# Kernel tuning notes

Measured on AMD Instinct MI355X. Metric: run time of the kernel, lower is better.

The kernel has to match this reference:

```python
import jax, jax.numpy as jnp
import numpy as np

N_NODES = 100000


def _gcn_layer(x, W, b, src, dst, inv_sqrt_deg):
    # transform first (cheaper when out_dim <= in_dim), then normalized aggregate
    h = x @ W  # [N, out]
    coeff = (inv_sqrt_deg[src] * inv_sqrt_deg[dst])[:, None]  # [E,1] sym norm
    msgs = h[src] * coeff  # [E, out]
    agg = jax.ops.segment_sum(msgs, dst, num_segments=N_NODES)  # [N, out]
    return agg + b


def setup_inputs() -> dict:
    key = jax.random.key(0)
    ks = jax.random.split(key, 8)
    n, e = N_NODES, 1600000
    x = jax.random.normal(ks[0], (n, 256), dtype=jnp.float32)
    src = jax.random.randint(ks[1], (e,), 0, n)
    dst = jax.random.randint(ks[2], (e,), 0, n)
    W1 = jax.random.normal(ks[3], (256, 128), dtype=jnp.float32) * 0.05
    b1 = jax.random.normal(ks[4], (128,), dtype=jnp.float32) * 0.05
    W2 = jax.random.normal(ks[5], (128, 40), dtype=jnp.float32) * 0.05
    b2 = jax.random.normal(ks[6], (40,), dtype=jnp.float32) * 0.05
    return {"x": x, "src": src, "dst": dst, "W1": W1, "b1": b1, "W2": W2, "b2": b2}


def reference(x, src, dst, W1, b1, W2, b2):
    # degree-based symmetric normalization D^{-1/2} A D^{-1/2}
    ones = jnp.ones(src.shape, dtype=x.dtype)
    deg = jax.ops.segment_sum(ones, dst, num_segments=N_NODES)
    inv_sqrt_deg = jnp.where(deg > 0, jax.lax.rsqrt(jnp.maximum(deg, 1.0)), 0.0)
    h = _gcn_layer(x, W1, b1, src, dst, inv_sqrt_deg)
    h = jax.nn.relu(h)
    h = _gcn_layer(h, W2, b2, src, dst, inv_sqrt_deg)
    return h
```

## Files before the change

### kernel.cpp

```cpp
#include <hip/hip_runtime.h>
#include <hip/hip_bf16.h>


#define CHUNK   4096
#define NPB     512
#define NBUCK   196
#define BBCAP   9216

typedef __bf16 bf16x8 __attribute__((ext_vector_type(8)));
typedef float floatx4 __attribute__((ext_vector_type(4)));

__device__ inline unsigned short f2bf(float f) {
    unsigned u = __float_as_uint(f);
    u += 0x7FFF + ((u >> 16) & 1);
    return (unsigned short)(u >> 16);
}
__device__ inline float bflo(unsigned p) { return __uint_as_float(p << 16); }
__device__ inline float bfhi(unsigned p) { return __uint_as_float(p & 0xFFFF0000u); }

__global__ __launch_bounds__(256) void k_f1(const int* __restrict__ src,
                                            const int* __restrict__ dst,
                                            int* __restrict__ gcursor,
                                            unsigned* __restrict__ buckets,
                                            int E, int nchunk,
                                            const float* __restrict__ W1,
                                            unsigned short* __restrict__ w1s,
                                            unsigned* __restrict__ h2z) {
    int t = threadIdx.x;
    if ((int)blockIdx.x >= nchunk) {
        int pb = blockIdx.x - nchunk;
        if (pb == 0 && t < 36) h2z[t] = 0;
        int flat = pb * 256 + t;
        int kt = flat >> 9;
        int nt = (flat >> 6) & 7;
        int lane = flat & 63;
        int kbase = kt * 32 + ((lane >> 4) << 3);
        int n = nt * 16 + (lane & 15);
        unsigned short v[8];
        #pragma unroll
        for (int j = 0; j < 8; ++j) v[j] = f2bf(W1[(size_t)(kbase + j) * 128 + n]);
        unsigned short* d = &w1s[(size_t)flat * 8];
        *(short4*)(d)     = make_short4(v[0], v[1], v[2], v[3]);
        *(short4*)(d + 4) = make_short4(v[4], v[5], v[6], v[7]);
        return;
    }
    __shared__ unsigned srec[CHUNK];
    __shared__ unsigned char sb8[CHUNK];
    __shared__ int hist[NBUCK];
    __shared__ int lbase[NBUCK];
    __shared__ int gbase[NBUCK];
    __shared__ int scanbuf[256];
    int base = blockIdx.x * CHUNK;
    int cnt = min(CHUNK, E - base);
    for (int i = t; i < NBUCK; i += 256) hist[i] = 0;
    __syncthreads();

    unsigned rec[16];
    unsigned br[16];
    bool valid[4];
    #pragma unroll
    for (int k = 0; k < 4; ++k) {
        int e0 = k * 1024 + t * 4;
        valid[k] = (e0 < cnt);
        if (valid[k]) {
            int4 s4 = *(const int4*)&src[base + e0];
            int4 d4 = *(const int4*)&dst[base + e0];
            int ss[4] = {s4.x, s4.y, s4.z, s4.w};
            int dd[4] = {d4.x, d4.y, d4.z, d4.w};
            #pragma unroll
            for (int j = 0; j < 4; ++j) {
                int b = dd[j] >> 9;
                int r = atomicAdd(&hist[b], 1);
                rec[k * 4 + j] = (unsigned)ss[j] | ((unsigned)(dd[j] & 511) << 17);
                br[k * 4 + j] = (unsigned)b | ((unsigned)r << 8);
            }
        }
    }
    __syncthreads();
    scanbuf[t] = (t < NBUCK) ? hist[t] : 0;
    __syncthreads();
    for (int s = 1; s < 256; s <<= 1) {
        int v = (t >= s) ? scanbuf[t - s] : 0;
        __syncthreads();
        scanbuf[t] += v;
        __syncthreads();
    }
    if (t < NBUCK) {
        lbase[t] = scanbuf[t] - hist[t];
        gbase[t] = atomicAdd(&gcursor[t], hist[t]);
    }
    __syncthreads();
    #pragma unroll
    for (int k = 0; k < 4; ++k) {
        if (valid[k]) {
            #pragma unroll
            for (int j = 0; j < 4; ++j) {
                unsigned b = br[k * 4 + j] & 255u;
                unsigned r = br[k * 4 + j] >> 8;
                int p = lbase[b] + (int)r;
                srec[p] = rec[k * 4 + j];
                sb8[p] = (unsigned char)b;
            }
        }
    }
    __syncthreads();
    for (int i = t; i < cnt; i += 256) {
        int b = sb8[i];
        int pos = gbase[b] + (i - lbase[b]);
        if (pos < BBCAP) buckets[(size_t)b * BBCAP + pos] = srec[i];
    }
}

__global__ __launch_bounds__(256) void k_f2(const unsigned* __restrict__ buckets,
                                            const int* __restrict__ gcursor,
                                            int* __restrict__ deg,
                                            int* __restrict__ counter,
                                            int* __restrict__ offsets,
                                            float* __restrict__ isd,
                                            int* __restrict__ csr,
                                            const float* __restrict__ X,
                                            const unsigned short* __restrict__ w1s,
                                            unsigned short* __restrict__ H, int N) {
    __shared__ __align__(16) unsigned char SH[16384];
    int tid = threadIdx.x;
    if ((int)blockIdx.x < NBUCK) {
        int* s_deg = (int*)SH;
        int* s_off = (int*)(SH + 2048);
        int* cur   = (int*)(SH + 4096);
        int* sb    = (int*)(SH + 6144);
        int* sbase = (int*)(SH + 7168);
        int b = blockIdx.x;
        int node0 = b << 9;
        int cnt = min(gcursor[b], BBCAP);
        const unsigned* bk = &buckets[(size_t)b * BBCAP];
        for (int i = tid; i < NPB; i += 256) s_deg[i] = 0;
        __syncthreads();
        for (int i = tid; i < cnt; i += 256)
            atomicAdd(&s_deg[bk[i] >> 17], 1);
        __syncthreads();
        int i0 = tid * 2;
        int na = node0 + i0, nb = node0 + i0 + 1;
        int da = s_deg[i0], db = s_deg[i0 + 1];
        if (na >= N) da = 0;
        if (nb >= N) db = 0;
        int dpa = (da + 15) & ~15, dpb = (db + 15) & ~15;
        sb[tid] = dpa + dpb;
        __syncthreads();
        for (int s = 1; s < 256; s <<= 1) {
            int v = (tid >= s) ? sb[tid - s] : 0;
            __syncthreads();
            sb[tid] += v;
            __syncthreads();
        }
        int excl = sb[tid] - (dpa + dpb);
        if (tid == 0) *sbase = atomicAdd(counter, sb[255]);
        if (b == 0 && tid == 1) isd[N] = 0.f;
        __syncthreads();
        int offa = *sbase + excl;
        int offb = offa + dpa;
        if (na < N) {
            deg[na] = da; offsets[na] = offa;
            isd[na] = (da > 0) ? rsqrtf((float)da) : 0.f;
        }
        if (nb < N) {
            deg[nb] = db; offsets[nb] = offb;
            isd[nb] = (db > 0) ? rsqrtf((float)db) : 0.f;
        }
        s_off[i0] = offa; s_off[i0 + 1] = offb;
        s_deg[i0] = da;   s_deg[i0 + 1] = db;
        cur[i0] = offa;   cur[i0 + 1] = offb;
        __syncthreads();
        for (int i = tid; i < cnt; i += 256) {
            unsigned r = bk[i];
            int p = atomicAdd(&cur[r >> 17], 1);
            csr[p] = (int)(r & 0x1FFFFu);
        }
        __syncthreads();
        for (int i = tid; i < NPB; i += 256) {
            int n = node0 + i;
            if (n < N) {
                int d = s_deg[i];
                int st = s_off[i] + d;
                int en = s_off[i] + ((d + 15) & ~15);
                for (int p = st; p < en; ++p) csr[p] = N;
            }
        }
        return;
    }
    unsigned short* smem = (unsigned short*)SH;
    unsigned short* sA = smem;
    unsigned short* sB = smem + 2048;
    int lane = tid & 63;
    int wave = tid >> 6;
    int wr = wave >> 1;
    int wc = wave & 1;
    int m0 = (blockIdx.x - NBUCK) * 64;

    floatx4 acc[2][4] = {};

    for (int kt = 0; kt < 8; ++kt) {
        #pragma unroll
        for (int i = 0; i < 2; ++i) {
            int f = tid * 2 + i;
            int row = f >> 3;
            int c4 = (f & 7) * 4;
            float4 v = make_float4(0.f, 0.f, 0.f, 0.f);
            int grow = m0 + row;
            if (grow < N) v = *(const float4*)&X[(size_t)grow * 256 + kt * 32 + c4];
            int mt = row >> 4;
            int flane = (row & 15) | ((c4 >> 3) << 4);
            int j0 = c4 & 7;
            unsigned short* d = &sA[(size_t)(mt * 64 + flane) * 8 + j0];
            *(short4*)d = make_short4(f2bf(v.x), f2bf(v.y), f2bf(v.z), f2bf(v.w));
        }
        {
            const float4* srcp = (const float4*)&w1s[(size_t)kt * 4096];
            float4* dstp = (float4*)sB;
            dstp[tid] = srcp[tid];
            dstp[tid + 256] = srcp[tid + 256];
        }
        __syncthreads();
        bf16x8 a[2], b[4];
        #pragma unroll
        for (int p = 0; p < 2; ++p)
            a[p] = *(const bf16x8*)&sA[(size_t)((wr * 2 + p) * 64 + lane) * 8];
        #pragma unroll
        for (int q = 0; q < 4; ++q)
            b[q] = *(const bf16x8*)&sB[(size_t)((wc * 4 + q) * 64 + lane) * 8];
        #pragma unroll
        for (int p = 0; p < 2; ++p)
            #pragma unroll
            for (int q = 0; q < 4; ++q)
                acc[p][q] = __builtin_amdgcn_mfma_f32_16x16x32_bf16(a[p], b[q], acc[p][q], 0, 0, 0);
        __syncthreads();
    }
    #pragma unroll
    for (int p = 0; p < 2; ++p)
        #pragma unroll
        for (int q = 0; q < 4; ++q)
            #pragma unroll
            for (int r = 0; r < 4; ++r) {
                int rl = wr * 32 + p * 16 + ((lane >> 4) << 2) + r;
                int c = wc * 64 + q * 16 + (lane & 15);
                smem[rl * 128 + c] = f2bf(acc[p][q][r]);
            }
    __syncthreads();
    #pragma unroll
    for (int i = 0; i < 4; ++i) {
        int f = tid + i * 256;
        int row = f >> 4;
        int c8 = (f & 15) * 8;
        int grow = m0 + row;
        if (grow <= N)
            *(float4*)&H[(size_t)grow * 128 + c8] = *(const float4*)&smem[row * 128 + c8];
    }
}

__global__ __launch_bounds__(256) void k_agg1(const unsigned* __restrict__ Hu,
                                              const int* __restrict__ csr,
                                              const float* __restrict__ isd,
                                              const int* __restrict__ offsets,
                                              const int* __restrict__ deg,
                                              const float* __restrict__ b1,
                                              unsigned* __restrict__ H1u, int N) {
    int node = __builtin_amdgcn_readfirstlane((blockIdx.x * blockDim.x + threadIdx.x) >> 6);
    int lane = threadIdx.x & 63;
    if (node >= N) return;
    int start = offsets[node];
    int nb = (deg[node] + 15) >> 4;
    float isdn = isd[node];
    float acc0 = 0.f, acc1 = 0.f;
    for (int ib = 0; ib < nb; ++ib) {
        int b0 = start + ib * 16;
        int s[16];
        #pragma unroll
        for (int j = 0; j < 16; ++j) s[j] = csr[b0 + j];
        float iss[16];
        #pragma unroll
        for (int j = 0; j < 16; ++j) iss[j] = isd[s[j]];
        unsigned p[16];
        #pragma unroll
        for (int j = 0; j < 16; ++j) p[j] = Hu[(size_t)s[j] * 64 + lane];
        #pragma unroll
        for (int j = 0; j < 16; ++j) {
            acc0 = fmaf(iss[j], bflo(p[j]), acc0);
            acc1 = fmaf(iss[j], bfhi(p[j]), acc1);
        }
    }
    float r0 = fmaxf(fmaf(isdn, acc0, b1[2 * lane]), 0.f);
    float r1 = fmaxf(fmaf(isdn, acc1, b1[2 * lane + 1]), 0.f);
    H1u[(size_t)node * 64 + lane] = (unsigned)f2bf(r0) | ((unsigned)f2bf(r1) << 16);
}

__global__ __launch_bounds__(256) void k_gemm2(const unsigned short* __restrict__ H1,
                                               const float* __restrict__ W2,
                                               const float* __restrict__ isd,
                                               unsigned short* __restrict__ H2, int N) {
    __shared__ float sH[64][132];
    __shared__ float sW[128 * 40];
    int tid = threadIdx.x;
    int block_row = blockIdx.x * 64;
    for (int i = tid; i < 64 * 16; i += 256) {
        int r = i >> 4;
        int c8 = (i & 15) * 8;
        int grow = block_row + r;
        uint4 v = make_uint4(0, 0, 0, 0);
        if (grow < N) v = *(const uint4*)&H1[(size_t)grow * 128 + c8];
        float* d = &sH[r][c8];
        d[0] = bflo(v.x); d[1] = bfhi(v.x);
        d[2] = bflo(v.y); d[3] = bfhi(v.y);
        d[4] = bflo(v.z); d[5] = bfhi(v.z);
        d[6] = bflo(v.w); d[7] = bfhi(v.w);
    }
    for (int i = tid; i < 1280; i += 256)
        *(float4*)&sW[i * 4] = *(const float4*)&W2[(size_t)i * 4];
    __syncthreads();

    int row = tid >> 2;
    int c0 = (tid & 3) * 10;
    float acc[10] = {};
    for (int k = 0; k < 128; ++k) {
        float hv = sH[row][k];
        #pragma unroll
        for (int j = 0; j < 5; ++j) {
            float2 wv = *(const float2*)&sW[k * 40 + c0 + 2 * j];
            acc[2 * j]     = fmaf(hv, wv.x, acc[2 * j]);
            acc[2 * j + 1] = fmaf(hv, wv.y, acc[2 * j + 1]);
        }
    }
    int grow = block_row + row;
    if (grow < N) {
        float scn = isd[grow];
        unsigned* o = (unsigned*)&H2[(size_t)grow * 40 + c0];
        #pragma unroll
        for (int j = 0; j < 5; ++j)
            o[j] = (unsigned)f2bf(acc[2 * j] * scn) |
                   ((unsigned)f2bf(acc[2 * j + 1] * scn) << 16);
    }
}

__global__ __launch_bounds__(256) void k_agg2(const unsigned* __restrict__ Hu2,
                                              const int* __restrict__ csr,
                                              const float* __restrict__ isd,
                                              const int* __restrict__ offsets,
                                              const int* __restrict__ deg,
                                              const float* __restrict__ b2,
                                              float* __restrict__ out, int N) {
    int node = __builtin_amdgcn_readfirstlane((blockIdx.x * blockDim.x + threadIdx.x) >> 6);
    int lane = threadIdx.x & 63;
    if (node >= N) return;
    int start = offsets[node];
    int nb = (deg[node] + 15) >> 4;
    float isdn = isd[node];
    int sub = lane >> 5;
    int c = lane & 31;
    float acc0 = 0.f, acc1 = 0.f;
    for (int ib = 0; ib < nb; ++ib) {
        int b0 = start + ib * 16;
        #pragma unroll
        for (int j = 0; j < 8; ++j) {
            int s = csr[b0 + (j << 1) + sub];
            unsigned q = Hu2[(size_t)s * 20 + c];
            acc0 += bflo(q);
            acc1 += bfhi(q);
        }
    }
    acc0 += __shfl(acc0, lane + 32);
    acc1 += __shfl(acc1, lane + 32);
    if (lane < 20)
        *(float2*)&out[(size_t)node * 40 + 2 * lane] =
            make_float2(fmaf(isdn, acc0, b2[2 * lane]), fmaf(isdn, acc1, b2[2 * lane + 1]));
}

extern "C" void kernel_launch(void* const* d_in, const int* in_sizes, int n_in,
                              void* d_out, int out_size, void* d_ws, size_t ws_size,
                              hipStream_t stream) {
    const float* x  = (const float*)d_in[0];
    const int*  src = (const int*)d_in[1];
    const int*  dst = (const int*)d_in[2];
    const float* W1 = (const float*)d_in[3];
    const float* b1 = (const float*)d_in[4];
    const float* W2 = (const float*)d_in[5];
    const float* b2 = (const float*)d_in[6];
    float* out = (float*)d_out;

    const int N = in_sizes[0] / 256;
    const int E = in_sizes[1];

    char* w = (char*)d_ws;
    auto alloc = [&](size_t bytes) -> void* {
        void* p = (void*)w;
        w += (bytes + 15) & ~(size_t)15;
        return p;
    };
    int*      gcursor = (int*)alloc(256 * 4);
    int*      counter = (int*)alloc(16);
    int*      deg     = (int*)alloc((size_t)N * 4);
    float*    isd     = (float*)alloc((size_t)(N + 1) * 4);
    int*      offsets = (int*)alloc((size_t)(N + 1) * 4);
    unsigned* buckets = (unsigned*)alloc((size_t)NBUCK * BBCAP * 4);
    int*      csr     = (int*)alloc((size_t)(E + 16 * (size_t)N) * 4);
    unsigned short* w1s = (unsigned short*)alloc(32768 * 2);
    unsigned short* h   = (unsigned short*)alloc((size_t)(N + 1) * 128 * 2);
    unsigned short* h1  = (unsigned short*)alloc((size_t)N * 128 * 2);
    unsigned short* h2  = (unsigned short*)alloc(((size_t)(N + 1) * 20 + 16) * 4);

    hipMemsetAsync(gcursor, 0, 256 * 4 + 16, stream);

    int nchunk = (E + CHUNK - 1) / CHUNK;
    int G1 = (N + 63) / 64;
    k_f1<<<nchunk + 16, 256, 0, stream>>>(src, dst, gcursor, buckets, E, nchunk,
                                          W1, w1s, (unsigned*)h2 + (size_t)N * 20);
    k_f2<<<NBUCK + G1, 256, 0, stream>>>(buckets, gcursor, deg, counter, offsets, isd,
                                         csr, x, w1s, h, N);
    k_agg1<<<(N + 3) / 4, 256, 0, stream>>>((const unsigned*)h, csr, isd, offsets, deg,
                                            b1, (unsigned*)h1, N);
    k_gemm2<<<G1, 256, 0, stream>>>(h1, W2, isd, h2, N);
    k_agg2<<<(N + 3) / 4, 256, 0, stream>>>((const unsigned*)h2, csr, isd, offsets, deg,
                                            b2, out, N);
}
```

Baseline: 374.9 us.

## Fuse layer-1 aggregation with layer-2 GEMM in one kernel

Merges the first-layer neighbour aggregation and the 128x40 second-layer transform into a single kernel. Each wave aggregates one node, writes its ReLU'd row to shared memory and immediately computes the 40 outputs against a transposed W2 held in LDS. This removes the bf16 H1 round trip through global memory and one kernel launch. The cost is loading W2 into LDS in every 1024-thread block, a larger LDS footprint that may lower occupancy, and only 40 of 64 lanes doing useful work in the dot-product step.

```diff
diff --git a/kernel.cpp b/kernel.cpp
--- a/kernel.cpp
+++ b/kernel.cpp
@@ -256,19 +256,40 @@
     }
 }
 
-__global__ __launch_bounds__(256) void k_agg1(const unsigned* __restrict__ Hu,
-                                              const int* __restrict__ csr,
-                                              const float* __restrict__ isd,
-                                              const int* __restrict__ offsets,
-                                              const int* __restrict__ deg,
-                                              const float* __restrict__ b1,
-                                              unsigned* __restrict__ H1u, int N) {
-    int node = __builtin_amdgcn_readfirstlane((blockIdx.x * blockDim.x + threadIdx.x) >> 6);
-    int lane = threadIdx.x & 63;
-    if (node >= N) return;
-    int start = offsets[node];
-    int nb = (deg[node] + 15) >> 4;
-    float isdn = isd[node];
+__global__ __launch_bounds__(1024) void k_agg1g2(const unsigned* __restrict__ Hu,
+                                                 const int* __restrict__ csr,
+                                                 const float* __restrict__ isd,
+                                                 const int* __restrict__ offsets,
+                                                 const int* __restrict__ deg,
+                                                 const float* __restrict__ b1,
+                                                 const float* __restrict__ W2,
+                                                 unsigned short* __restrict__ H2s,
+                                                 int N) {
+    __shared__ float sW2t[40 * 133];
+    __shared__ float h1row[16 * 128];
+    int tid = threadIdx.x;
+    for (int j = tid; j < 1280; j += 1024) {
+        float4 v = *(const float4*)&W2[(size_t)j * 4];
+        int c0 = (4 * j) % 40;
+        int k  = (4 * j) / 40;
+        sW2t[(c0 + 0) * 133 + k] = v.x;
+        sW2t[(c0 + 1) * 133 + k] = v.y;
+        sW2t[(c0 + 2) * 133 + k] = v.z;
+        sW2t[(c0 + 3) * 133 + k] = v.w;
+    }
+    __syncthreads();
+
+    int wv = tid >> 6;
+    int lane = tid & 63;
+    int node = __builtin_amdgcn_readfirstlane(blockIdx.x * 16 + wv);
+    bool live = (node < N);
+    int start = 0, nb = 0;
+    float isdn = 0.f;
+    if (live) {
+        start = offsets[node];
+        nb = (deg[node] + 15) >> 4;
+        isdn = isd[node];
+    }
     float acc0 = 0.f, acc1 = 0.f;
     for (int ib = 0; ib < nb; ++ib) {
         int b0 = start + ib * 16;
@@ -289,54 +310,23 @@
     }
     float r0 = fmaxf(fmaf(isdn, acc0, b1[2 * lane]), 0.f);
     float r1 = fmaxf(fmaf(isdn, acc1, b1[2 * lane + 1]), 0.f);
-    H1u[(size_t)node * 64 + lane] = (unsigned)f2bf(r0) | ((unsigned)f2bf(r1) << 16);
-}
-
-__global__ __launch_bounds__(256) void k_gemm2(const unsigned short* __restrict__ H1,
-                                               const float* __restrict__ W2,
-                                               const float* __restrict__ isd,
-                                               unsigned short* __restrict__ H2, int N) {
-    __shared__ float sH[64][132];
-    __shared__ float sW[128 * 40];
-    int tid = threadIdx.x;
-    int block_row = blockIdx.x * 64;
-    for (int i = tid; i < 64 * 16; i += 256) {
-        int r = i >> 4;
-        int c8 = (i & 15) * 8;
-        int grow = block_row + r;
-        uint4 v = make_uint4(0, 0, 0, 0);
-        if (grow < N) v = *(const uint4*)&H1[(size_t)grow * 128 + c8];
-        float* d = &sH[r][c8];
-        d[0] = bflo(v.x); d[1] = bfhi(v.x);
-        d[2] = bflo(v.y); d[3] = bfhi(v.y);
-        d[4] = bflo(v.z); d[5] = bfhi(v.z);
-        d[6] = bflo(v.w); d[7] = bfhi(v.w);
-    }
-    for (int i = tid; i < 1280; i += 256)
-        *(float4*)&sW[i * 4] = *(const float4*)&W2[(size_t)i * 4];
-    __syncthreads();
-
-    int row = tid >> 2;
-    int c0 = (tid & 3) * 10;
-    float acc[10] = {};
-    for (int k = 0; k < 128; ++k) {
-        float hv = sH[row][k];
-        #pragma unroll
-        for (int j = 0; j < 5; ++j) {
-            float2 wv = *(const float2*)&sW[k * 40 + c0 + 2 * j];
-            acc[2 * j]     = fmaf(hv, wv.x, acc[2 * j]);
-            acc[2 * j + 1] = fmaf(hv, wv.y, acc[2 * j + 1]);
-        }
-    }
-    int grow = block_row + row;
-    if (grow < N) {
-        float scn = isd[grow];
-        unsigned* o = (unsigned*)&H2[(size_t)grow * 40 + c0];
-        #pragma unroll
-        for (int j = 0; j < 5; ++j)
-            o[j] = (unsigned)f2bf(acc[2 * j] * scn) |
-                   ((unsigned)f2bf(acc[2 * j + 1] * scn) << 16);
-    }
+    float* hr = &h1row[wv * 128];
+    *(float2*)&hr[2 * lane] = make_float2(r0, r1);
+    asm volatile("s_waitcnt lgkmcnt(0)" ::: "memory");
+    int cc = (lane < 40) ? lane : 0;
+    const float* wcol = &sW2t[cc * 133];
+    float s0 = 0.f, s1 = 0.f, s2 = 0.f, s3 = 0.f;
+    #pragma unroll
+    for (int kb = 0; kb < 32; ++kb) {
+        float4 hv = *(const float4*)&hr[kb * 4];
+        s0 = fmaf(hv.x, wcol[4 * kb + 0], s0);
+        s1 = fmaf(hv.y, wcol[4 * kb + 1], s1);
+        s2 = fmaf(hv.z, wcol[4 * kb + 2], s2);
+        s3 = fmaf(hv.w, wcol[4 * kb + 3], s3);
+    }
+    float hv2 = (s0 + s1) + (s2 + s3);
+    if (live && lane < 40)
+        H2s[(size_t)node * 40 + lane] = f2bf(hv2 * isdn);
 }
 
 __global__ __launch_bounds__(256) void k_agg2(const unsigned* __restrict__ Hu2,
@@ -402,7 +392,6 @@
     int*      csr     = (int*)alloc((size_t)(E + 16 * (size_t)N) * 4);
     unsigned short* w1s = (unsigned short*)alloc(32768 * 2);
     unsigned short* h   = (unsigned short*)alloc((size_t)(N + 1) * 128 * 2);
-    unsigned short* h1  = (unsigned short*)alloc((size_t)N * 128 * 2);
     unsigned short* h2  = (unsigned short*)alloc(((size_t)(N + 1) * 20 + 16) * 4);
 
     hipMemsetAsync(gcursor, 0, 256 * 4 + 16, stream);
@@ -413,9 +402,8 @@
                                           W1, w1s, (unsigned*)h2 + (size_t)N * 20);
     k_f2<<<NBUCK + G1, 256, 0, stream>>>(buckets, gcursor, deg, counter, offsets, isd,
                                          csr, x, w1s, h, N);
-    k_agg1<<<(N + 3) / 4, 256, 0, stream>>>((const unsigned*)h, csr, isd, offsets, deg,
-                                            b1, (unsigned*)h1, N);
-    k_gemm2<<<G1, 256, 0, stream>>>(h1, W2, isd, h2, N);
+    k_agg1g2<<<(N + 15) / 16, 1024, 0, stream>>>((const unsigned*)h, csr, isd, offsets,
+                                                 deg, b1, W2, h2, N);
     k_agg2<<<(N + 3) / 4, 256, 0, stream>>>((const unsigned*)h2, csr, isd, offsets, deg,
                                             b2, out, N);
 }
```

Result: no change. 382.4 us (+2.0%).

## Use bf16 MFMA with split-W2 hi/lo terms for second-layer GEMM

Applied to the files above, without the earlier changes.

Replaces the scalar FP32 FMA loop in the second-layer transform with MFMA 16x16x32 bf16 instructions. W2 is split into high and low bf16 parts, pre-swizzled into MFMA fragment layout by extra blocks in the first kernel, so accuracy stays close to FP32 weights. H1 tiles are staged in LDS in fragment order, and the output goes through an LDS staging buffer for coalesced 16-byte stores. The aim is to cut ALU time and LDS traffic in k_gemm2, at the cost of padding 40 columns to 48 and doing two MFMAs per tile.

```diff
diff --git a/kernel.cpp b/kernel.cpp
--- a/kernel.cpp
+++ b/kernel.cpp
@@ -25,8 +25,33 @@
                                             int E, int nchunk,
                                             const float* __restrict__ W1,
                                             unsigned short* __restrict__ w1s,
+                                            const float* __restrict__ W2,
+                                            unsigned short* __restrict__ w2f,
                                             unsigned* __restrict__ h2z) {
     int t = threadIdx.x;
+    if ((int)blockIdx.x >= nchunk + 16) {
+        int flat2 = (blockIdx.x - nchunk - 16) * 256 + t;
+        int term = flat2 >= 768;
+        int u = term ? flat2 - 768 : flat2;
+        int kt = u / 192;
+        int rm = u - kt * 192;
+        int nt = rm >> 6;
+        int lane = rm & 63;
+        unsigned short vv[8];
+        #pragma unroll
+        for (int j = 0; j < 8; ++j) {
+            int k = kt * 32 + ((lane >> 4) << 3) + j;
+            int c = nt * 16 + (lane & 15);
+            float wv = (c < 40) ? W2[(size_t)k * 40 + c] : 0.f;
+            unsigned short hi = f2bf(wv);
+            if (term == 0) vv[j] = hi;
+            else vv[j] = f2bf(wv - __uint_as_float((unsigned)hi << 16));
+        }
+        unsigned short* d = &w2f[(size_t)flat2 * 8];
+        *(short4*)(d)     = make_short4(vv[0], vv[1], vv[2], vv[3]);
+        *(short4*)(d + 4) = make_short4(vv[4], vv[5], vv[6], vv[7]);
+        return;
+    }
     if ((int)blockIdx.x >= nchunk) {
         int pb = blockIdx.x - nchunk;
         if (pb == 0 && t < 36) h2z[t] = 0;
@@ -293,49 +318,58 @@
 }
 
 __global__ __launch_bounds__(256) void k_gemm2(const unsigned short* __restrict__ H1,
-                                               const float* __restrict__ W2,
+                                               const unsigned short* __restrict__ w2f,
                                                const float* __restrict__ isd,
-                                               unsigned short* __restrict__ H2, int N) {
-    __shared__ float sH[64][132];
-    __shared__ float sW[128 * 40];
+                                               unsigned short* __restrict__ H2s, int N) {
+    __shared__ __align__(16) unsigned short sA[8192];
+    __shared__ __align__(16) unsigned short sC[64 * 56];
     int tid = threadIdx.x;
     int block_row = blockIdx.x * 64;
-    for (int i = tid; i < 64 * 16; i += 256) {
-        int r = i >> 4;
-        int c8 = (i & 15) * 8;
-        int grow = block_row + r;
+    #pragma unroll
+    for (int i = 0; i < 4; ++i) {
+        int f = tid + i * 256;
+        int row = f >> 4;
+        int c8 = (f & 15) * 8;
         uint4 v = make_uint4(0, 0, 0, 0);
+        int grow = block_row + row;
         if (grow < N) v = *(const uint4*)&H1[(size_t)grow * 128 + c8];
-        float* d = &sH[r][c8];
-        d[0] = bflo(v.x); d[1] = bfhi(v.x);
-        d[2] = bflo(v.y); d[3] = bfhi(v.y);
-        d[4] = bflo(v.z); d[5] = bfhi(v.z);
-        d[6] = bflo(v.w); d[7] = bfhi(v.w);
-    }
-    for (int i = tid; i < 1280; i += 256)
-        *(float4*)&sW[i * 4] = *(const float4*)&W2[(size_t)i * 4];
-    __syncthreads();
-
-    int row = tid >> 2;
-    int c0 = (tid & 3) * 10;
-    float acc[10] = {};
-    for (int k = 0; k < 128; ++k) {
-        float hv = sH[row][k];
-        #pragma unroll
-        for (int j = 0; j < 5; ++j) {
-            float2 wv = *(const float2*)&sW[k * 40 + c0 + 2 * j];
-            acc[2 * j]     = fmaf(hv, wv.x, acc[2 * j]);
-            acc[2 * j + 1] = fmaf(hv, wv.y, acc[2 * j + 1]);
-        }
-    }
-    int grow = block_row + row;
-    if (grow < N) {
-        float scn = isd[grow];
-        unsigned* o = (unsigned*)&H2[(size_t)grow * 40 + c0];
-        #pragma unroll
-        for (int j = 0; j < 5; ++j)
-            o[j] = (unsigned)f2bf(acc[2 * j] * scn) |
-                   ((unsigned)f2bf(acc[2 * j + 1] * scn) << 16);
+        int kt = c8 >> 5;
+        int g  = (c8 >> 3) & 3;
+        int mt = row >> 4;
+        *(uint4*)&sA[(size_t)((((kt << 2) + mt) << 6) + ((row & 15) | (g << 4))) * 8] = v;
+    }
+    __syncthreads();
+    int wr = tid >> 6;
+    int lane = tid & 63;
+    floatx4 acc[3] = {};
+    #pragma unroll
+    for (int kt = 0; kt < 4; ++kt) {
+        bf16x8 a = *(const bf16x8*)&sA[(size_t)((((kt << 2) + wr) << 6) + lane) * 8];
+        #pragma unroll
+        for (int nt = 0; nt < 3; ++nt) {
+            bf16x8 bh = *(const bf16x8*)&w2f[(size_t)((kt * 3 + nt) * 64 + lane) * 8];
+            bf16x8 bl = *(const bf16x8*)&w2f[(size_t)(768 + (kt * 3 + nt) * 64 + lane) * 8];
+            acc[nt] = __builtin_amdgcn_mfma_f32_16x16x32_bf16(a, bh, acc[nt], 0, 0, 0);
+            acc[nt] = __builtin_amdgcn_mfma_f32_16x16x32_bf16(a, bl, acc[nt], 0, 0, 0);
+        }
+    }
+    #pragma unroll
+    for (int r = 0; r < 4; ++r) {
+        int row = wr * 16 + ((lane >> 4) << 2) + r;
+        int g = block_row + row;
+        float sc = isd[g > N ? N : g];
+        #pragma unroll
+        for (int nt = 0; nt < 3; ++nt)
+            sC[row * 56 + nt * 16 + (lane & 15)] = f2bf(acc[nt][r] * sc);
+    }
+    __syncthreads();
+    if (tid < 64) {
+        int grow = block_row + tid;
+        if (grow < N) {
+            #pragma unroll
+            for (int j = 0; j < 5; ++j)
+                *(uint4*)&H2s[(size_t)grow * 40 + j * 8] = *(const uint4*)&sC[tid * 56 + j * 8];
+        }
     }
 }
 
@@ -401,6 +435,7 @@
     unsigned* buckets = (unsigned*)alloc((size_t)NBUCK * BBCAP * 4);
     int*      csr     = (int*)alloc((size_t)(E + 16 * (size_t)N) * 4);
     unsigned short* w1s = (unsigned short*)alloc(32768 * 2);
+    unsigned short* w2f = (unsigned short*)alloc(12288 * 2);
     unsigned short* h   = (unsigned short*)alloc((size_t)(N + 1) * 128 * 2);
     unsigned short* h1  = (unsigned short*)alloc((size_t)N * 128 * 2);
     unsigned short* h2  = (unsigned short*)alloc(((size_t)(N + 1) * 20 + 16) * 4);
@@ -409,13 +444,14 @@
 
     int nchunk = (E + CHUNK - 1) / CHUNK;
     int G1 = (N + 63) / 64;
-    k_f1<<<nchunk + 16, 256, 0, stream>>>(src, dst, gcursor, buckets, E, nchunk,
-                                          W1, w1s, (unsigned*)h2 + (size_t)N * 20);
+    k_f1<<<nchunk + 22, 256, 0, stream>>>(src, dst, gcursor, buckets, E, nchunk,
+                                          W1, w1s, W2, w2f,
+                                          (unsigned*)h2 + (size_t)N * 20);
     k_f2<<<NBUCK + G1, 256, 0, stream>>>(buckets, gcursor, deg, counter, offsets, isd,
                                          csr, x, w1s, h, N);
     k_agg1<<<(N + 3) / 4, 256, 0, stream>>>((const unsigned*)h, csr, isd, offsets, deg,
                                             b1, (unsigned*)h1, N);
-    k_gemm2<<<G1, 256, 0, stream>>>(h1, W2, isd, h2, N);
+    k_gemm2<<<G1, 256, 0, stream>>>(h1, w2f, isd, h2, N);
     k_agg2<<<(N + 3) / 4, 256, 0, stream>>>((const unsigned*)h2, csr, isd, offsets, deg,
                                             b2, out, N);
 }
```

Measured after the change: 345.2 us, median of 2. -7.9%, faster.
